# Performance work log

Measured on AMD Instinct MI355X. Metric: run time of the kernel, lower is better.

The kernel has to match this reference:

```python
import jax, jax.numpy as jnp
import numpy as np
import math

RADIUS = 1.0
PERCENTAGES = (0.02, 0.04, 0.06, 0.08, 0.10)


def _fps(pts, npoint):
    """Furthest point sampling. pts: [N,3] -> idx [npoint] int32 (starts at index 0,
    matching pointnet2 CUDA furthest_point_sample)."""
    N = pts.shape[0]

    def step(carry, _):
        dists, last = carry
        d = jnp.sum((pts - pts[last]) ** 2, axis=-1)
        dists = jnp.minimum(dists, d)
        nxt = jnp.argmax(dists).astype(jnp.int32)
        return (dists, nxt), nxt

    init = (jnp.full((N,), 1e10, pts.dtype), jnp.int32(0))
    _, rest = jax.lax.scan(step, init, None, length=npoint - 1)
    return jnp.concatenate([jnp.zeros((1,), jnp.int32), rest])


def _ball_query(pcd, queries, r, nsample):
    """pcd [B,N,3], queries [B,M,3] -> idx [B,M,nsample] int32.
    First (by index order) points with squared dist < r^2; groups with fewer than
    nsample in-radius points are padded with the first found index (pn2 semantics)."""
    N = pcd.shape[1]
    d2 = jnp.sum((queries[:, :, None, :] - pcd[:, None, :, :]) ** 2, axis=-1)  # [B,M,N]
    key = jnp.where(d2 < r * r, jnp.arange(N, dtype=jnp.int32), jnp.int32(N))
    srt = jnp.sort(key, axis=-1)[:, :, :nsample]  # first in-radius indices
    valid = srt < N
    first = jnp.where(srt[:, :, :1] < N, srt[:, :, :1], 0)
    return jnp.where(valid, srt, first)


def _nn_dist(g):
    """g [G,n,3] -> [G,n] distance to nearest neighbor (2nd-smallest pairwise
    Euclidean distance, i.e. KNN(k=2) dist[:,:,1] including self-distance 0)."""
    sq = jnp.sum(g * g, axis=-1)  # [G,n]
    d2 = sq[:, :, None] + sq[:, None, :] - 2.0 * jnp.einsum('gnc,gmc->gnm', g, g)
    d2 = jnp.maximum(d2, 0.0)
    # safe sqrt (zero grad at exact zeros: self / duplicated padded points)
    d = jnp.where(d2 > 0, jnp.sqrt(jnp.where(d2 > 0, d2, 1.0)), 0.0)
    neg2, _ = jax.lax.top_k(-d, 2)  # two smallest distances
    return -neg2[:, :, 1]


def _uniform_loss(pcd):
    B, N, C = pcd.shape
    npoint = int(N * 0.05)
    fps_idx = jax.vmap(_fps, in_axes=(0, None))(pcd, npoint)  # [B,M]
    new_xyz = jnp.take_along_axis(pcd, fps_idx[:, :, None], axis=1)  # [B,M,3]
    loss = jnp.zeros((), pcd.dtype)
    for p in PERCENTAGES:
        nsample = int(N * p)
        r = math.sqrt(p * RADIUS)
        disk_area = math.pi * RADIUS ** 2 / N
        expect_len = math.sqrt(disk_area)
        idx = _ball_query(pcd, new_xyz, r, nsample)  # [B,M,n]
        grouped = jax.vmap(lambda pts, ii: pts[ii])(pcd, idx)  # [B,M,n,3]
        g = grouped.reshape(B * npoint, nsample, C)
        nn = _nn_dist(g)  # [G,n]
        e_ = 0.1
        u = jnp.abs(nn + e_)
        u = jnp.mean(u, axis=1)  # [G]
        u = (u - expect_len) ** 2 / (expect_len + e_)
        loss = loss + jnp.mean(u) * (p * 100.0) ** 2
    return loss / len(PERCENTAGES)


def setup_inputs() -> dict:
    key = jax.random.key(0)
    pcd = jax.random.uniform(key, (2, 4096, 3), dtype=jnp.float32)
    return {"pcd": pcd}


def reference(pcd):
    return _uniform_loss(pcd)
```

## Files before the change

kernel.cpp:

```cpp
#include <hip/hip_runtime.h>
#include <cmath>

#define NPTS 4096
#define NPOINT 204
#define NPCT 5
#define MAXNS 409
#define FPS_T 256
#define NGROUP 408
#define NPART (NGROUP * NPCT)
#define MAXSLOT 7

typedef unsigned long long u64;
typedef float f32x2 __attribute__((ext_vector_type(2)));

struct LossParams {
    int   nsample[NPCT];
    float r2[NPCT];
    float wscale[NPCT];
    float expect_len;
};

template <int CTRL>
__device__ __forceinline__ int dpp_imax(int v) {
    int t = __builtin_amdgcn_update_dpp(0, v, CTRL, 0xf, 0xf, true);
    return v > t ? v : t;
}
template <int CTRL>
__device__ __forceinline__ int dpp_imin(int v) {
    int t = __builtin_amdgcn_update_dpp(0x7fffffff, v, CTRL, 0xf, 0xf, false);
    return v < t ? v : t;
}
__device__ __forceinline__ int wave_max_i(int v) {
    v = dpp_imax<0x111>(v); v = dpp_imax<0x112>(v);
    v = dpp_imax<0x114>(v); v = dpp_imax<0x118>(v);
    v = dpp_imax<0x142>(v); v = dpp_imax<0x143>(v);
    return __builtin_amdgcn_readlane(v, 63);
}
__device__ __forceinline__ int wave_min_i(int v) {
    v = dpp_imin<0x111>(v); v = dpp_imin<0x112>(v);
    v = dpp_imin<0x114>(v); v = dpp_imin<0x118>(v);
    v = dpp_imin<0x142>(v); v = dpp_imin<0x143>(v);
    return __builtin_amdgcn_readlane(v, 63);
}
template <int CTRL>
__device__ __forceinline__ u64 dpp_u64max(u64 v) {
    int lo = (int)(unsigned)v;
    int hi = (int)(unsigned)(v >> 32);
    unsigned slo = (unsigned)__builtin_amdgcn_update_dpp(0, lo, CTRL, 0xf, 0xf, true);
    unsigned shi = (unsigned)__builtin_amdgcn_update_dpp(0, hi, CTRL, 0xf, 0xf, true);
    u64 o = ((u64)shi << 32) | slo;
    return v > o ? v : o;
}

__global__ __launch_bounds__(FPS_T) void fps_kernel(const float* __restrict__ pcd,
                                                    int* __restrict__ fps_idx) {
#pragma clang fp contract(off)
    __shared__ float4 pts[NPTS];
    __shared__ u64 keys[2][4];

    const int b = blockIdx.x;
    const int t = threadIdx.x;
    const int wave = t >> 6, lane = t & 63;
    const float* base = pcd + (size_t)b * NPTS * 3;

    f32x2 X[8], Y[8], Z[8], D[8];
    #pragma unroll
    for (int q = 0; q < 8; ++q) {
        int n0 = (2 * q) * FPS_T + t;
        int n1 = (2 * q + 1) * FPS_T + t;
        float x0 = base[3 * n0 + 0], y0 = base[3 * n0 + 1], z0 = base[3 * n0 + 2];
        float x1 = base[3 * n1 + 0], y1 = base[3 * n1 + 1], z1 = base[3 * n1 + 2];
        pts[n0] = make_float4(x0, y0, z0, 0.0f);
        pts[n1] = make_float4(x1, y1, z1, 0.0f);
        X[q] = (f32x2){x0, x1};
        Y[q] = (f32x2){y0, y1};
        Z[q] = (f32x2){z0, z1};
        D[q] = (f32x2){1e10f, 1e10f};
    }
    int* out = fps_idx + b * NPOINT;
    if (t == 0) out[0] = 0;
    __syncthreads();

    float4 c = pts[0];
    for (int it = 1; it < NPOINT; ++it) {
        f32x2 cxx = (f32x2){c.x, c.x};
        f32x2 cyy = (f32x2){c.y, c.y};
        f32x2 czz = (f32x2){c.z, c.z};
        int bb = -1, bi = 0;
        #pragma unroll
        for (int q = 0; q < 8; ++q) {
            f32x2 dx = X[q] - cxx, dy = Y[q] - cyy, dz = Z[q] - czz;
            f32x2 d  = (dx * dx + dy * dy) + dz * dz;
            f32x2 dd = D[q];
            float d0 = fminf(dd.x, d.x);
            float d1 = fminf(dd.y, d.y);
            D[q] = (f32x2){d0, d1};
            int b0 = __float_as_int(d0);
            int b1 = __float_as_int(d1);
            if (b0 > bb) { bb = b0; bi = (2 * q) * FPS_T + t; }
            if (b1 > bb) { bb = b1; bi = (2 * q + 1) * FPS_T + t; }
        }
        int wmax = wave_max_i(bb);
        int cand = (bb == wmax) ? bi : 0x7fffffff;
        int widx = wave_min_i(cand);
        if (lane == 0)
            keys[it & 1][wave] =
                ((u64)(unsigned)wmax << 32) | (unsigned)~(unsigned)widx;
        __syncthreads();
        u64 kv = keys[it & 1][lane & 3];
        kv = dpp_u64max<0x111>(kv);
        kv = dpp_u64max<0x112>(kv);
        unsigned lo3 = (unsigned)__builtin_amdgcn_readlane((int)(unsigned)kv, 3);
        int last = (int)~lo3;
        c = pts[last];
        if (t == 0) out[it] = last;
    }
}

template <int K>
__device__ __forceinline__ void phaseB(const float4* __restrict__ gpts,
                                       float2 (*wres)[64],
                                       int j0, int j1, int lane, int cntB) {
    float4 pi[K];
    float m1[K], m2[K];
    #pragma unroll
    for (int s = 0; s < K; ++s) {
        int idx = s * 64 + lane;
        pi[s] = gpts[idx < cntB ? idx : 0];
        m1[s] = 1e30f; m2[s] = 1e30f;
    }
    #pragma unroll 2
    for (int j = j0; j < j1; ++j) {
        float4 a = gpts[j];
        #pragma unroll
        for (int s = 0; s < K; ++s) {
            float tt = pi[s].x * a.x;
            tt = fmaf(pi[s].y, a.y, tt);
            tt = fmaf(pi[s].z, a.z, tt);
            float h = fmaf(-2.0f, tt, a.w);
            m2[s] = __builtin_amdgcn_fmed3f(m1[s], m2[s], h);
            m1[s] = fminf(m1[s], h);
        }
    }
    #pragma unroll
    for (int s = 0; s < K; ++s) wres[s][lane] = (float2){m1[s], m2[s]};
}

__global__ __launch_bounds__(256) void group_kernel(const float* __restrict__ pcd,
                                                    const int* __restrict__ fps_idx,
                                                    float* __restrict__ partials,
                                                    LossParams P) {
    const int xid  = blockIdx.x;
    const int pidx = xid % NPCT;
    const int g    = xid / NPCT;
    const int b    = g / NPOINT;
    const int m    = g - b * NPOINT;
    const int t    = threadIdx.x;
    const int wave = t >> 6, lane = t & 63;

    const int   ns = P.nsample[pidx];
    const float r2 = P.r2[pidx];

    __shared__ float4 gpts[MAXNS];
    __shared__ float2 wres[4][MAXSLOT][64];
    __shared__ int    s_wtot[4];
    __shared__ float  s_part[4];

    const float* base = pcd + (size_t)b * NPTS * 3;
    int qi = fps_idx[b * NPOINT + m];
    float qx = base[3 * qi + 0], qy = base[3 * qi + 1], qz = base[3 * qi + 2];

    unsigned long long msk[16];
    int lbase[16];
    int run = 0;
    #pragma unroll 4
    for (int s = 0; s < 16; ++s) {
        int n = wave * 1024 + s * 64 + lane;
        float x = base[3 * n + 0];
        float y = base[3 * n + 1];
        float z = base[3 * n + 2];
        float d2;
        {
#pragma clang fp contract(off)
            float dx = qx - x, dy = qy - y, dz = qz - z;
            float aa = dx * dx, bb = dy * dy, cc = dz * dz;
            d2 = (aa + bb) + cc;
        }
        msk[s] = __ballot(d2 < r2);
        lbase[s] = run;
        run += __popcll(msk[s]);
    }
    if (lane == 0) s_wtot[wave] = run;
    __syncthreads();
    int w0 = s_wtot[0], w1 = s_wtot[1], w2 = s_wtot[2], w3 = s_wtot[3];
    int Bw = (wave > 0 ? w0 : 0) + (wave > 1 ? w1 : 0) + (wave > 2 ? w2 : 0);
    int cnt  = w0 + w1 + w2 + w3;
    int cntB = cnt < ns ? cnt : ns;
    const int npad = ns - cntB;

    #pragma unroll 4
    for (int s = 0; s < 16; ++s) {
        int gb = Bw + lbase[s];
        if (gb >= ns) break;
        unsigned long long mk = msk[s];
        bool in = (mk >> lane) & 1ull;
        int pos = gb + __popcll(mk & ((1ull << lane) - 1ull));
        if (in && pos < ns) {
            int n = wave * 1024 + s * 64 + lane;
            float x = base[3 * n], y = base[3 * n + 1], z = base[3 * n + 2];
            float sq = fmaf(x, x, fmaf(y, y, z * z));
            gpts[pos] = make_float4(x, y, z, sq);
        }
    }
    __syncthreads();

    const int quarter = (cntB + 3) >> 2;
    const int j0 = wave * quarter;
    const int j1 = (j0 + quarter) < cntB ? (j0 + quarter) : cntB;
    const int nslot = (cntB + 63) >> 6;
    switch (nslot) {
        case 1: phaseB<1>(gpts, wres[wave], j0, j1, lane, cntB); break;
        case 2: phaseB<2>(gpts, wres[wave], j0, j1, lane, cntB); break;
        case 3: phaseB<3>(gpts, wres[wave], j0, j1, lane, cntB); break;
        case 4: phaseB<4>(gpts, wres[wave], j0, j1, lane, cntB); break;
        case 5: phaseB<5>(gpts, wres[wave], j0, j1, lane, cntB); break;
        case 6: phaseB<6>(gpts, wres[wave], j0, j1, lane, cntB); break;
        default: phaseB<7>(gpts, wres[wave], j0, j1, lane, cntB); break;
    }
    __syncthreads();

    float sum = 0.0f;
    for (int it = t; it < nslot * 64; it += 256) {
        int i = it;
        if (i < cntB) {
            int s = it >> 6, l = it & 63;
            float2 a = wres[0][s][l];
            float2 bq = wres[1][s][l];
            float2 cq = wres[2][s][l];
            float2 dq = wres[3][s][l];
            float e1 = fminf(a.x, bq.x), e2 = fminf(fmaxf(a.x, bq.x), fminf(a.y, bq.y));
            float f1 = fminf(cq.x, dq.x), f2 = fminf(fmaxf(cq.x, dq.x), fminf(cq.y, dq.y));
            float m2v = fminf(fmaxf(e1, f1), fminf(e2, f2));
            float sq = gpts[i].w;
            float d2 = fmaxf(sq + m2v, 0.0f);
            if (!(i == 0 && npad > 0)) sum += sqrtf(d2);
        }
    }
    #pragma unroll
    for (int off = 32; off; off >>= 1) sum += __shfl_down(sum, off);
    if (lane == 0) s_part[wave] = sum;
    __syncthreads();
    if (t == 0) {
        float tot = s_part[0] + s_part[1] + s_part[2] + s_part[3] + 0.1f * (float)ns;
        float u  = tot / (float)ns;
        float du = u - P.expect_len;
        partials[xid] = du * du / (P.expect_len + 0.1f) * P.wscale[pidx];
    }
}

__global__ __launch_bounds__(256) void reduce_kernel(const float* __restrict__ partials,
                                                     float* __restrict__ out) {
    const int t = threadIdx.x;
    __shared__ float sp[4];
    float s = 0.0f;
    for (int i = t; i < NPART; i += 256) s += partials[i];
    #pragma unroll
    for (int off = 32; off; off >>= 1) s += __shfl_down(s, off);
    if ((t & 63) == 0) sp[t >> 6] = s;
    __syncthreads();
    if (t == 0) out[0] = sp[0] + sp[1] + sp[2] + sp[3];
}

extern "C" void kernel_launch(void* const* d_in, const int* in_sizes, int n_in,
                              void* d_out, int out_size, void* d_ws, size_t ws_size,
                              hipStream_t stream) {
    const float* pcd = (const float*)d_in[0];
    const int B = in_sizes[0] / (NPTS * 3);
    float* out = (float*)d_out;
    int*   fps = (int*)d_ws;
    float* partials = (float*)d_ws + NGROUP;

    fps_kernel<<<dim3(B), dim3(FPS_T), 0, stream>>>(pcd, fps);

    LossParams P;
    const double ps[NPCT] = {0.02, 0.04, 0.06, 0.08, 0.10};
    for (int i = 0; i < NPCT; ++i) {
        P.nsample[i] = (int)(NPTS * ps[i]);
        double r = std::sqrt(ps[i] * 1.0);
        P.r2[i] = (float)(r * r);
        double w = (ps[i] * 100.0) * (ps[i] * 100.0);
        P.wscale[i] = (float)(w / (double)(B * NPOINT * NPCT));
    }
    P.expect_len = (float)std::sqrt(3.14159265358979323846 / (double)NPTS);

    group_kernel<<<dim3(NPART), dim3(256), 0, stream>>>(pcd, fps, partials, P);
    reduce_kernel<<<dim3(1), dim3(256), 0, stream>>>(partials, out);
}
```

Before: 213.9 us.

## Fuse FPS and grouping into one persistent kernel with flag-based streaming

Merges the FPS and group kernels into one launch. Two blocks run furthest-point sampling and publish each sampled index with an atomic store. 510 persistent worker blocks spin-wait on a -1 sentinel, set by a memset, and process groups in FPS order, so ball query and NN work overlap the long serial FPS loop. The FPS blocks get raised wave priority. The design relies on all blocks being co-resident to avoid deadlock, and adds spin-polling and a memset launch.

```diff
diff --git a/kernel.cpp b/kernel.cpp
--- a/kernel.cpp
+++ b/kernel.cpp
@@ -10,6 +10,16 @@
 #define NPART (NGROUP * NPCT)
 #define MAXSLOT 7
 
+#define NWORK  510
+#define NROUND 4
+
+#define SMEM_BYTES 65600
+#define KEYS_OFF   65536
+#define WRES_OFF   6544
+#define WTOT_OFF   20880
+#define SPART_OFF  20896
+#define SQI_OFF    20912
+
 typedef unsigned long long u64;
 typedef float f32x2 __attribute__((ext_vector_type(2)));
 
@@ -52,11 +62,13 @@
     return v > o ? v : o;
 }
 
-__global__ __launch_bounds__(FPS_T) void fps_kernel(const float* __restrict__ pcd,
-                                                    int* __restrict__ fps_idx) {
+__device__ void fps_role(const float* __restrict__ pcd,
+                         int* __restrict__ fps_idx,
+                         char* smem) {
 #pragma clang fp contract(off)
-    __shared__ float4 pts[NPTS];
-    __shared__ u64 keys[2][4];
+    __builtin_amdgcn_s_setprio(3);
+    float4* pts = reinterpret_cast<float4*>(smem);
+    u64 (*keys)[4] = reinterpret_cast<u64 (*)[4]>(smem + KEYS_OFF);
 
     const int b = blockIdx.x;
     const int t = threadIdx.x;
@@ -78,7 +90,8 @@
         D[q] = (f32x2){1e10f, 1e10f};
     }
     int* out = fps_idx + b * NPOINT;
-    if (t == 0) out[0] = 0;
+    if (t == 0)
+        __hip_atomic_store(&out[0], 0, __ATOMIC_RELAXED, __HIP_MEMORY_SCOPE_AGENT);
     __syncthreads();
 
     float4 c = pts[0];
@@ -113,7 +126,8 @@
         unsigned lo3 = (unsigned)__builtin_amdgcn_readlane((int)(unsigned)kv, 3);
         int last = (int)~lo3;
         c = pts[last];
-        if (t == 0) out[it] = last;
+        if (t == 0)
+            __hip_atomic_store(&out[it], last, __ATOMIC_RELAXED, __HIP_MEMORY_SCOPE_AGENT);
     }
 }
 
@@ -146,115 +160,141 @@
     for (int s = 0; s < K; ++s) wres[s][lane] = (float2){m1[s], m2[s]};
 }
 
-__global__ __launch_bounds__(256) void group_kernel(const float* __restrict__ pcd,
-                                                    const int* __restrict__ fps_idx,
-                                                    float* __restrict__ partials,
-                                                    LossParams P) {
-    const int xid  = blockIdx.x;
-    const int pidx = xid % NPCT;
-    const int g    = xid / NPCT;
-    const int b    = g / NPOINT;
-    const int m    = g - b * NPOINT;
-    const int t    = threadIdx.x;
+__device__ void worker_role(const float* __restrict__ pcd,
+                            int* __restrict__ fps_idx,
+                            float* __restrict__ partials,
+                            const LossParams& P, char* smem) {
+    float4* gpts = reinterpret_cast<float4*>(smem);
+    auto wres    = reinterpret_cast<float2 (*)[MAXSLOT][64]>(smem + WRES_OFF);
+    int*   s_wtot = reinterpret_cast<int*>(smem + WTOT_OFF);
+    float* s_part = reinterpret_cast<float*>(smem + SPART_OFF);
+    int*   s_qi   = reinterpret_cast<int*>(smem + SQI_OFF);
+
+    const int w = blockIdx.x - 2;
+    const int t = threadIdx.x;
     const int wave = t >> 6, lane = t & 63;
 
-    const int   ns = P.nsample[pidx];
-    const float r2 = P.r2[pidx];
-
-    __shared__ float4 gpts[MAXNS];
-    __shared__ float2 wres[4][MAXSLOT][64];
-    __shared__ int    s_wtot[4];
-    __shared__ float  s_part[4];
-
-    const float* base = pcd + (size_t)b * NPTS * 3;
-    int qi = fps_idx[b * NPOINT + m];
-    float qx = base[3 * qi + 0], qy = base[3 * qi + 1], qz = base[3 * qi + 2];
-
-    unsigned long long msk[16];
-    int lbase[16];
-    int run = 0;
-    #pragma unroll 4
-    for (int s = 0; s < 16; ++s) {
-        int n = wave * 1024 + s * 64 + lane;
-        float x = base[3 * n + 0];
-        float y = base[3 * n + 1];
-        float z = base[3 * n + 2];
-        float d2;
-        {
+    for (int round = 0; round < NROUND; ++round) {
+        const int tau  = w + round * NWORK;
+        const int m_   = tau / 10;
+        const int rem  = tau - m_ * 10;
+        const int b    = rem / 5;
+        const int pidx = rem - b * 5;
+
+        const int   ns = P.nsample[pidx];
+        const float r2 = P.r2[pidx];
+        const float* base = pcd + (size_t)b * NPTS * 3;
+
+        if (t == 0) {
+            int q;
+            while ((q = __hip_atomic_load(&fps_idx[b * NPOINT + m_],
+                                          __ATOMIC_RELAXED,
+                                          __HIP_MEMORY_SCOPE_AGENT)) < 0)
+                __builtin_amdgcn_s_sleep(16);
+            s_qi[0] = q;
+        }
+        __syncthreads();
+        const int qi = s_qi[0];
+        float qx = base[3 * qi + 0], qy = base[3 * qi + 1], qz = base[3 * qi + 2];
+
+        unsigned long long msk[16];
+        int lbase[16];
+        int run = 0;
+        #pragma unroll 4
+        for (int s = 0; s < 16; ++s) {
+            int n = wave * 1024 + s * 64 + lane;
+            float x = base[3 * n + 0];
+            float y = base[3 * n + 1];
+            float z = base[3 * n + 2];
+            float d2;
+            {
 #pragma clang fp contract(off)
-            float dx = qx - x, dy = qy - y, dz = qz - z;
-            float aa = dx * dx, bb = dy * dy, cc = dz * dz;
-            d2 = (aa + bb) + cc;
-        }
-        msk[s] = __ballot(d2 < r2);
-        lbase[s] = run;
-        run += __popcll(msk[s]);
-    }
-    if (lane == 0) s_wtot[wave] = run;
-    __syncthreads();
-    int w0 = s_wtot[0], w1 = s_wtot[1], w2 = s_wtot[2], w3 = s_wtot[3];
-    int Bw = (wave > 0 ? w0 : 0) + (wave > 1 ? w1 : 0) + (wave > 2 ? w2 : 0);
-    int cnt  = w0 + w1 + w2 + w3;
-    int cntB = cnt < ns ? cnt : ns;
-    const int npad = ns - cntB;
-
-    #pragma unroll 4
-    for (int s = 0; s < 16; ++s) {
-        int gb = Bw + lbase[s];
-        if (gb >= ns) break;
-        unsigned long long mk = msk[s];
-        bool in = (mk >> lane) & 1ull;
-        int pos = gb + __popcll(mk & ((1ull << lane) - 1ull));
-        if (in && pos < ns) {
-            int n = wave * 1024 + s * 64 + lane;
-            float x = base[3 * n], y = base[3 * n + 1], z = base[3 * n + 2];
-            float sq = fmaf(x, x, fmaf(y, y, z * z));
-            gpts[pos] = make_float4(x, y, z, sq);
-        }
-    }
-    __syncthreads();
-
-    const int quarter = (cntB + 3) >> 2;
-    const int j0 = wave * quarter;
-    const int j1 = (j0 + quarter) < cntB ? (j0 + quarter) : cntB;
-    const int nslot = (cntB + 63) >> 6;
-    switch (nslot) {
-        case 1: phaseB<1>(gpts, wres[wave], j0, j1, lane, cntB); break;
-        case 2: phaseB<2>(gpts, wres[wave], j0, j1, lane, cntB); break;
-        case 3: phaseB<3>(gpts, wres[wave], j0, j1, lane, cntB); break;
-        case 4: phaseB<4>(gpts, wres[wave], j0, j1, lane, cntB); break;
-        case 5: phaseB<5>(gpts, wres[wave], j0, j1, lane, cntB); break;
-        case 6: phaseB<6>(gpts, wres[wave], j0, j1, lane, cntB); break;
-        default: phaseB<7>(gpts, wres[wave], j0, j1, lane, cntB); break;
-    }
-    __syncthreads();
-
-    float sum = 0.0f;
-    for (int it = t; it < nslot * 64; it += 256) {
-        int i = it;
-        if (i < cntB) {
-            int s = it >> 6, l = it & 63;
-            float2 a = wres[0][s][l];
-            float2 bq = wres[1][s][l];
-            float2 cq = wres[2][s][l];
-            float2 dq = wres[3][s][l];
-            float e1 = fminf(a.x, bq.x), e2 = fminf(fmaxf(a.x, bq.x), fminf(a.y, bq.y));
-            float f1 = fminf(cq.x, dq.x), f2 = fminf(fmaxf(cq.x, dq.x), fminf(cq.y, dq.y));
-            float m2v = fminf(fmaxf(e1, f1), fminf(e2, f2));
-            float sq = gpts[i].w;
-            float d2 = fmaxf(sq + m2v, 0.0f);
-            if (!(i == 0 && npad > 0)) sum += sqrtf(d2);
-        }
-    }
-    #pragma unroll
-    for (int off = 32; off; off >>= 1) sum += __shfl_down(sum, off);
-    if (lane == 0) s_part[wave] = sum;
-    __syncthreads();
-    if (t == 0) {
-        float tot = s_part[0] + s_part[1] + s_part[2] + s_part[3] + 0.1f * (float)ns;
-        float u  = tot / (float)ns;
-        float du = u - P.expect_len;
-        partials[xid] = du * du / (P.expect_len + 0.1f) * P.wscale[pidx];
+                float dx = qx - x, dy = qy - y, dz = qz - z;
+                float aa = dx * dx, bb = dy * dy, cc = dz * dz;
+                d2 = (aa + bb) + cc;
+            }
+            msk[s] = __ballot(d2 < r2);
+            lbase[s] = run;
+            run += __popcll(msk[s]);
+        }
+        if (lane == 0) s_wtot[wave] = run;
+        __syncthreads();
+        int w0 = s_wtot[0], w1 = s_wtot[1], w2 = s_wtot[2], w3 = s_wtot[3];
+        int Bw = (wave > 0 ? w0 : 0) + (wave > 1 ? w1 : 0) + (wave > 2 ? w2 : 0);
+        int cnt  = w0 + w1 + w2 + w3;
+        int cntB = cnt < ns ? cnt : ns;
+        const int npad = ns - cntB;
+
+        #pragma unroll 4
+        for (int s = 0; s < 16; ++s) {
+            int gb = Bw + lbase[s];
+            if (gb >= ns) break;
+            unsigned long long mk = msk[s];
+            bool in = (mk >> lane) & 1ull;
+            int pos = gb + __popcll(mk & ((1ull << lane) - 1ull));
+            if (in && pos < ns) {
+                int n = wave * 1024 + s * 64 + lane;
+                float x = base[3 * n], y = base[3 * n + 1], z = base[3 * n + 2];
+                float sq = fmaf(x, x, fmaf(y, y, z * z));
+                gpts[pos] = make_float4(x, y, z, sq);
+            }
+        }
+        __syncthreads();
+
+        const int quarter = (cntB + 3) >> 2;
+        const int j0 = wave * quarter;
+        const int j1 = (j0 + quarter) < cntB ? (j0 + quarter) : cntB;
+        const int nslot = (cntB + 63) >> 6;
+        switch (nslot) {
+            case 1: phaseB<1>(gpts, wres[wave], j0, j1, lane, cntB); break;
+            case 2: phaseB<2>(gpts, wres[wave], j0, j1, lane, cntB); break;
+            case 3: phaseB<3>(gpts, wres[wave], j0, j1, lane, cntB); break;
+            case 4: phaseB<4>(gpts, wres[wave], j0, j1, lane, cntB); break;
+            case 5: phaseB<5>(gpts, wres[wave], j0, j1, lane, cntB); break;
+            case 6: phaseB<6>(gpts, wres[wave], j0, j1, lane, cntB); break;
+            default: phaseB<7>(gpts, wres[wave], j0, j1, lane, cntB); break;
+        }
+        __syncthreads();
+
+        float sum = 0.0f;
+        for (int it = t; it < nslot * 64; it += 256) {
+            int i = it;
+            if (i < cntB) {
+                int s = it >> 6, l = it & 63;
+                float2 a  = wres[0][s][l];
+                float2 bq = wres[1][s][l];
+                float2 cq = wres[2][s][l];
+                float2 dq = wres[3][s][l];
+                float e1 = fminf(a.x, bq.x), e2 = fminf(fmaxf(a.x, bq.x), fminf(a.y, bq.y));
+                float f1 = fminf(cq.x, dq.x), f2 = fminf(fmaxf(cq.x, dq.x), fminf(cq.y, dq.y));
+                float m2v = fminf(fmaxf(e1, f1), fminf(e2, f2));
+                float sq = gpts[i].w;
+                float d2 = fmaxf(sq + m2v, 0.0f);
+                if (!(i == 0 && npad > 0)) sum += sqrtf(d2);
+            }
+        }
+        #pragma unroll
+        for (int off = 32; off; off >>= 1) sum += __shfl_down(sum, off);
+        if (lane == 0) s_part[wave] = sum;
+        __syncthreads();
+        if (t == 0) {
+            float tot = s_part[0] + s_part[1] + s_part[2] + s_part[3] + 0.1f * (float)ns;
+            float u  = tot / (float)ns;
+            float du = u - P.expect_len;
+            partials[tau] = du * du / (P.expect_len + 0.1f) * P.wscale[pidx];
+        }
+    }
+}
+
+__global__ __launch_bounds__(256, 2) void fused_kernel(const float* __restrict__ pcd,
+                                                       int* __restrict__ fps_idx,
+                                                       float* __restrict__ partials,
+                                                       LossParams P) {
+    __shared__ __align__(16) char smem[SMEM_BYTES];
+    if (blockIdx.x < 2) {
+        fps_role(pcd, fps_idx, smem);
+    } else {
+        worker_role(pcd, fps_idx, partials, P, smem);
     }
 }
 
@@ -280,7 +320,7 @@
     int*   fps = (int*)d_ws;
     float* partials = (float*)d_ws + NGROUP;
 
-    fps_kernel<<<dim3(B), dim3(FPS_T), 0, stream>>>(pcd, fps);
+    hipMemsetAsync(fps, 0xFF, NGROUP * sizeof(int), stream);
 
     LossParams P;
     const double ps[NPCT] = {0.02, 0.04, 0.06, 0.08, 0.10};
@@ -293,6 +333,6 @@
     }
     P.expect_len = (float)std::sqrt(3.14159265358979323846 / (double)NPTS);
 
-    group_kernel<<<dim3(NPART), dim3(256), 0, stream>>>(pcd, fps, partials, P);
+    fused_kernel<<<dim3(2 + NWORK), dim3(256), 0, stream>>>(pcd, fps, partials, P);
     reduce_kernel<<<dim3(1), dim3(256), 0, stream>>>(partials, out);
 }
```

After: 187.8 us. 12.2% less time.
